# Kernel optimization log

Hardware: AMD Instinct MI355X
Metric: run time of the kernel (lower is better)

The kernel has to match this reference:

```python
import jax, jax.numpy as jnp
import numpy as np

DIM = 1024
HEADS = 16
HIDDEN = 4 * DIM


def layernorm(x, g, b, eps=1e-5):
    mu = jnp.mean(x, axis=-1, keepdims=True)
    var = jnp.mean(jnp.square(x - mu), axis=-1, keepdims=True)
    return (x - mu) * jax.lax.rsqrt(var + eps) * g + b


def setup_inputs() -> dict:
    key = jax.random.key(0)
    ks = jax.random.split(key, 8)
    s = DIM ** -0.5
    return {
        "x": jax.random.normal(ks[0], (2, 2048, DIM), dtype=jnp.float32),
        "ln1_g": jnp.ones((DIM,), jnp.float32),
        "ln1_b": jnp.zeros((DIM,), jnp.float32),
        "qkv_w": jax.random.normal(ks[1], (DIM, 3 * DIM), jnp.float32) * s,
        "proj_w": jax.random.normal(ks[2], (DIM, DIM), jnp.float32) * s,
        "proj_b": jnp.zeros((DIM,), jnp.float32),
        "ln2_g": jnp.ones((DIM,), jnp.float32),
        "ln2_b": jnp.zeros((DIM,), jnp.float32),
        "fc1_w": jax.random.normal(ks[3], (DIM, HIDDEN), jnp.float32) * s,
        "fc1_b": jnp.zeros((HIDDEN,), jnp.float32),
        "fc2_w": jax.random.normal(ks[4], (HIDDEN, DIM), jnp.float32) * (HIDDEN ** -0.5),
        "fc2_b": jnp.zeros((DIM,), jnp.float32),
    }


def block_fwd(x, ln1_g, ln1_b, qkv_w, proj_w, proj_b, ln2_g, ln2_b,
              fc1_w, fc1_b, fc2_w, fc2_b):
    B, N, C = x.shape
    H = HEADS
    Dh = C // H
    scale = Dh ** -0.5
    # --- attention branch (pre-norm) ---
    h = layernorm(x, ln1_g, ln1_b)
    qkv = h @ qkv_w                     # [B,N,3C] (no bias: qkv_bias=False)
    qkv = qkv.reshape(B, N, 3, H, Dh)
    q = qkv[:, :, 0].transpose(0, 2, 1, 3)   # [B,H,N,Dh]
    k = qkv[:, :, 1].transpose(0, 2, 1, 3)
    v = qkv[:, :, 2].transpose(0, 2, 1, 3)
    attn = jnp.einsum('bhqd,bhkd->bhqk', q, k) * scale
    attn = jax.nn.softmax(attn, axis=-1)
    o = jnp.einsum('bhqk,bhkd->bhqd', attn, v)
    o = o.transpose(0, 2, 1, 3).reshape(B, N, C)
    x = x + (o @ proj_w + proj_b)
    # --- MLP branch (pre-norm) ---
    h = layernorm(x, ln2_g, ln2_b)
    h = jax.nn.gelu(h @ fc1_w + fc1_b, approximate=False)  # torch nn.GELU = exact erf
    x = x + (h @ fc2_w + fc2_b)
    return x


def reference(x, ln1_g, ln1_b, qkv_w, proj_w, proj_b, ln2_g, ln2_b,
              fc1_w, fc1_b, fc2_w, fc2_b):
    return block_fwd(x, ln1_g, ln1_b, qkv_w, proj_w, proj_b, ln2_g, ln2_b,
                     fc1_w, fc1_b, fc2_w, fc2_b)
```

## Files before the change

### kernel.cpp

```cpp
#include <hip/hip_runtime.h>
#include <math.h>

typedef unsigned short u16;
typedef unsigned int u32;
typedef __attribute__((ext_vector_type(8))) short short8;
typedef __attribute__((ext_vector_type(4))) float f32x4;
typedef __attribute__((ext_vector_type(2))) u32 u32x2;
typedef __attribute__((ext_vector_type(4))) u32 u32x4;
typedef __attribute__((ext_vector_type(4))) u16 u16x4;

typedef __attribute__((address_space(1))) const void gmem_t;
typedef __attribute__((address_space(3))) void lmem_t;

__device__ __forceinline__ u16 f2bf(float f) {
  u32 u = __builtin_bit_cast(u32, f);
  u = u + 0x7fffu + ((u >> 16) & 1u);
  return (u16)(u >> 16);
}

__device__ __forceinline__ u32 cvt_pk_bf16(float a, float b) {
  u32 r;
  asm("v_cvt_pk_bf16_f32 %0, %1, %2" : "=v"(r) : "v"(a), "v"(b));
  return r;
}

__device__ __forceinline__ void g2l16(const void* g, void* l) {
  __builtin_amdgcn_global_load_lds((gmem_t*)g, (lmem_t*)l, 16, 0, 0);
}

template <int N> __device__ __forceinline__ void waitcnt_vm() {
  if constexpr (N == 0)      asm volatile("s_waitcnt vmcnt(0)" ::: "memory");
  else if constexpr (N == 4) asm volatile("s_waitcnt vmcnt(4)" ::: "memory");
  else if constexpr (N == 6) asm volatile("s_waitcnt vmcnt(6)" ::: "memory");
  else if constexpr (N == 8) asm volatile("s_waitcnt vmcnt(8)" ::: "memory");
  else static_assert(N == 0 || N == 4 || N == 6 || N == 8, "add literal");
}

__global__ __launch_bounds__(256) void wtrans_all(
    const float* __restrict__ qkvw, const float* __restrict__ projw,
    const float* __restrict__ fc1w, const float* __restrict__ fc2w,
    u16* __restrict__ o_qkv, u16* __restrict__ o_proj,
    u16* __restrict__ o_fc1, u16* __restrict__ o_fc2) {
  int id = (int)blockIdx.x;
  const float* in; u16* out; int R, C, bid;
  if (id < 768)       { in = qkvw;  out = o_qkv;  R = 1024; C = 3072; bid = id; }
  else if (id < 1024) { in = projw; out = o_proj; R = 1024; C = 1024; bid = id - 768; }
  else if (id < 2048) { in = fc1w;  out = o_fc1;  R = 1024; C = 4096; bid = id - 1024; }
  else                { in = fc2w;  out = o_fc2;  R = 4096; C = 1024; bid = id - 2048; }
  __shared__ float t[64][65];
  int tid = threadIdx.x;
  int nbx = C >> 6;
  int bx = bid % nbx, by = bid / nbx;
  int r0 = by << 6, c0 = bx << 6;
  int lr = tid >> 2, lc = (tid & 3) << 4;
  const float* src = in + (size_t)(r0 + lr) * C + c0 + lc;
#pragma unroll
  for (int j = 0; j < 4; ++j) {
    f32x4 v = *(const f32x4*)(src + j * 4);
    t[lr][lc + j * 4 + 0] = v.x; t[lr][lc + j * 4 + 1] = v.y;
    t[lr][lc + j * 4 + 2] = v.z; t[lr][lc + j * 4 + 3] = v.w;
  }
  __syncthreads();
  int oc = tid >> 2, orr = (tid & 3) << 4;
  u16* dst = out + (size_t)(c0 + oc) * R + r0 + orr;
  u32 u[8];
#pragma unroll
  for (int j = 0; j < 8; ++j)
    u[j] = (u32)f2bf(t[orr + 2 * j][oc]) | ((u32)f2bf(t[orr + 2 * j + 1][oc]) << 16);
  u32x4 v0; v0.x = u[0]; v0.y = u[1]; v0.z = u[2]; v0.w = u[3];
  u32x4 v1; v1.x = u[4]; v1.y = u[5]; v1.z = u[6]; v1.w = u[7];
  *(u32x4*)(dst) = v0;
  *(u32x4*)(dst + 8) = v1;
}

__global__ __launch_bounds__(256) void lnorm(const float* __restrict__ in,
                                             const float* __restrict__ gw,
                                             const float* __restrict__ bw,
                                             u16* __restrict__ out) {
  int r = blockIdx.x, tid = threadIdx.x;
  const f32x4 v = *((const f32x4*)(in + (size_t)r * 1024) + tid);
  float s = v.x + v.y + v.z + v.w;
  float ss = v.x * v.x + v.y * v.y + v.z * v.z + v.w * v.w;
#pragma unroll
  for (int o = 32; o >= 1; o >>= 1) { s += __shfl_xor(s, o); ss += __shfl_xor(ss, o); }
  __shared__ float red[8];
  int w = tid >> 6;
  if ((tid & 63) == 0) { red[w] = s; red[4 + w] = ss; }
  __syncthreads();
  s = red[0] + red[1] + red[2] + red[3];
  ss = red[4] + red[5] + red[6] + red[7];
  float mu = s * (1.0f / 1024.0f);
  float var = ss * (1.0f / 1024.0f) - mu * mu;
  float rstd = rsqrtf(var + 1e-5f);
  const f32x4 g4 = *((const f32x4*)gw + tid);
  const f32x4 b4 = *((const f32x4*)bw + tid);
  u16x4 o;
  o.x = f2bf((v.x - mu) * rstd * g4.x + b4.x);
  o.y = f2bf((v.y - mu) * rstd * g4.y + b4.y);
  o.z = f2bf((v.z - mu) * rstd * g4.z + b4.z);
  o.w = f2bf((v.w - mu) * rstd * g4.w + b4.w);
  *((u16x4*)(out + (size_t)r * 1024) + tid) = o;
}

template <int EPI, int BM, int BN>
__global__ __launch_bounds__(256, 2) void gemm_bt(
    const u16* __restrict__ A, const u16* __restrict__ BT, int M, int N, int K,
    const float* __restrict__ bias, const float* __restrict__ resid,
    float* __restrict__ fout, u16* __restrict__ bout,
    u16* __restrict__ bout2, u16* __restrict__ bout3) {
  constexpr int AIT = BM / 32, BIT = BN / 32;
  constexpr int L = AIT + BIT;
  constexpr int MR = BM / 32, NR = BN / 32;
  __shared__ __align__(16) u16 smA[2][BM * 64];
  __shared__ __align__(16) u16 smB[2][BN * 64];
  int tid = threadIdx.x;
  int w = tid >> 6, l = tid & 63, lq = l & 15, g = l >> 4;
  int nbx = N / BN;
  int t = (int)blockIdx.x;
  int cpx = (int)gridDim.x >> 3;
  t = (t & 7) * cpx + (t >> 3);
  int by = t / nbx, bx = t - by * nbx;
  long brow = (long)by * BM, bcol = (long)bx * BN;
  int wr = w >> 1, wc = w & 1;

  const u16* aS[AIT]; const u16* bS[BIT];
#pragma unroll
  for (int it = 0; it < AIT; ++it) {
    int p = it * 256 + tid;
    int row = p >> 3;
    int gc = (p & 7) ^ (row & 7);
    aS[it] = A + (size_t)(brow + row) * K + gc * 8;
  }
#pragma unroll
  for (int it = 0; it < BIT; ++it) {
    int p = it * 256 + tid;
    int row = p >> 3;
    int gc = (p & 7) ^ (row & 7);
    bS[it] = BT + (size_t)(bcol + row) * K + gc * 8;
  }
  auto STAGE = [&](int buf, int k0) {
#pragma unroll
    for (int it = 0; it < AIT; ++it) g2l16(aS[it] + k0, &smA[buf][it * 2048 + w * 512]);
#pragma unroll
    for (int it = 0; it < BIT; ++it) g2l16(bS[it] + k0, &smB[buf][it * 2048 + w * 512]);
  };

  f32x4 zero = {0.f, 0.f, 0.f, 0.f};
  f32x4 acc[MR][NR];
#pragma unroll
  for (int m = 0; m < MR; ++m)
#pragma unroll
    for (int n = 0; n < NR; ++n) acc[m][n] = zero;

  int NT = K >> 6;
  STAGE(0, 0);
  for (int tt = 0; tt < NT; ++tt) {
    int cur = tt & 1;
    int knext = ((tt + 1) == NT ? 0 : (tt + 1)) << 6;
    STAGE(cur ^ 1, knext);
    waitcnt_vm<L>();
    __builtin_amdgcn_s_barrier();
    asm volatile("" ::: "memory");

    const char* sA = (const char*)&smA[cur][0];
    const char* sB = (const char*)&smB[cur][0];
#pragma unroll
    for (int c = 0; c < 2; ++c) {
      short8 af[MR], bfb[NR];
#pragma unroll
      for (int m = 0; m < MR; ++m) {
        int r = wr * (BM / 2) + m * 16 + lq;
        af[m] = *(const short8*)(sA + r * 128 + ((g * 16 + c * 64) ^ ((r & 7) << 4)));
      }
#pragma unroll
      for (int n = 0; n < NR; ++n) {
        int r = wc * (BN / 2) + n * 16 + lq;
        bfb[n] = *(const short8*)(sB + r * 128 + ((g * 16 + c * 64) ^ ((r & 7) << 4)));
      }
#pragma unroll
      for (int m = 0; m < MR; ++m)
#pragma unroll
        for (int n = 0; n < NR; ++n)
          acc[m][n] = __builtin_amdgcn_mfma_f32_16x16x32_bf16(af[m], bfb[n], acc[m][n], 0, 0, 0);
    }
    asm volatile("" ::: "memory");
    __builtin_amdgcn_s_barrier();
  }
  waitcnt_vm<0>();

  long colbase = bcol + wc * (BN / 2);
#pragma unroll
  for (int m = 0; m < MR; ++m) {
#pragma unroll
    for (int n = 0; n < NR; ++n) {
      f32x4 v = acc[m][n];
      long col = colbase + n * 16 + lq;
      long row0 = brow + wr * (BM / 2) + m * 16 + g * 4;
      if constexpr (EPI == 0) {
        int part = (int)(bcol >> 10);
        long colq = col - ((long)part << 10);
        int hh = (int)(colq >> 6), d = (int)(colq & 63);
#pragma unroll
        for (int i = 0; i < 4; ++i) {
          long row = row0 + i;
          long b = row >> 11, nq = row & 2047;
          long bh = b * 16 + hh;
          u16 val = f2bf(v[i]);
          if (part == 0)      bout [(bh * 2048 + nq) * 64 + d] = val;
          else if (part == 1) bout2[(bh * 2048 + nq) * 64 + d] = val;
          else                bout3[(bh * 64 + d) * 2048 + nq] = val;
        }
      } else if constexpr (EPI == 1 || EPI == 3) {
        float bb = bias[col];
#pragma unroll
        for (int i = 0; i < 4; ++i) {
          long idx = (row0 + i) * N + col;
          fout[idx] = resid[idx] + v[i] + bb;
        }
      } else {
        float bb = bias[col];
#pragma unroll
        for (int i = 0; i < 4; ++i) {
          float xg = v[i] + bb;
          float ge = 0.5f * xg * (1.0f + erff(xg * 0.70710678118654752f));
          bout[(row0 + i) * N + col] = f2bf(ge);
        }
      }
    }
  }
}

__global__ __launch_bounds__(256, 4) void attn_fwd(const u16* __restrict__ qb,
                                                   const u16* __restrict__ kb,
                                                   const u16* __restrict__ vtb,
                                                   u16* __restrict__ ob) {
  __shared__ __align__(16) u16 kl[2][64 * 64];
  __shared__ __align__(16) u16 vl[2][64 * 64];
  __shared__ __align__(16) u16 pl[4][16 * 64];
  int tid = threadIdx.x;
  int w = tid >> 6, l = tid & 63, lq = l & 15, g = l >> 4;
  int bh = (int)blockIdx.x & 31;
  int qt = (int)blockIdx.x >> 5;

  const u16* qr = qb + ((size_t)bh * 2048 + qt * 64 + w * 16 + lq) * 64 + g * 8;
  short8 qf0 = *(const short8*)qr;
  short8 qf1 = *(const short8*)(qr + 32);

  const u16* kS[2]; const u16* vS[2];
#pragma unroll
  for (int it = 0; it < 2; ++it) {
    int p = it * 256 + tid;
    int row = p >> 3;
    int gc = (p & 7) ^ (row & 7);
    kS[it] = kb + ((size_t)bh * 2048 + row) * 64 + gc * 8;
    vS[it] = vtb + ((size_t)bh * 64 + row) * 2048 + gc * 8;
  }
  auto issue = [&](int buf, int kt0) {
#pragma unroll
    for (int it = 0; it < 2; ++it) {
      g2l16(kS[it] + (size_t)kt0 * 64, &kl[buf][it * 2048 + w * 512]);
      g2l16(vS[it] + kt0,              &vl[buf][it * 2048 + w * 512]);
    }
  };

  f32x4 zero = {0.f, 0.f, 0.f, 0.f};
  f32x4 accO[4] = {zero, zero, zero, zero};
  f32x4 accl = zero;
  const float sc = 0.125f * 1.44269504088896f;
  u32x4 ov; ov.x = ov.y = ov.z = ov.w = 0x3F803F80u;
  short8 onesf = __builtin_bit_cast(short8, ov);
  int plswz = (lq & 7) << 4;

  issue(0, 0);
  for (int t = 0; t < 32; ++t) {
    int cur = t & 1;
    issue(cur ^ 1, ((t + 1) & 31) << 6);
    waitcnt_vm<4>();
    __builtin_amdgcn_s_barrier();
    asm volatile("" ::: "memory");

    const char* klc = (const char*)&kl[cur][0];
    const char* vlc = (const char*)&vl[cur][0];

    f32x4 s[4];
    short8 ka0[4], ka1[4];
#pragma unroll
    for (int kt = 0; kt < 4; ++kt) {
      int r = kt * 16 + lq;
      ka0[kt] = *(const short8*)(klc + (r * 128 + ((g * 16) ^ ((r & 7) << 4))));
      ka1[kt] = *(const short8*)(klc + (r * 128 + ((g * 16 + 64) ^ ((r & 7) << 4))));
    }
    __builtin_amdgcn_s_setprio(1);
#pragma unroll
    for (int kt = 0; kt < 4; ++kt) {
      s[kt] = __builtin_amdgcn_mfma_f32_16x16x32_bf16(ka0[kt], qf0, zero, 0, 0, 0);
      s[kt] = __builtin_amdgcn_mfma_f32_16x16x32_bf16(ka1[kt], qf1, s[kt], 0, 0, 0);
    }
    __builtin_amdgcn_s_setprio(0);

    char* plw = (char*)&pl[w][0];
#pragma unroll
    for (int kt = 0; kt < 4; ++kt) {
      u32x2 uu;
      uu.x = cvt_pk_bf16(exp2f(s[kt][0] * sc - 12.0f), exp2f(s[kt][1] * sc - 12.0f));
      uu.y = cvt_pk_bf16(exp2f(s[kt][2] * sc - 12.0f), exp2f(s[kt][3] * sc - 12.0f));
      *(u32x2*)(plw + ((lq * 128 + kt * 32 + g * 8) ^ plswz)) = uu;
    }

#pragma unroll
    for (int c = 0; c < 2; ++c) {
      short8 pa = *(const short8*)(plw + ((lq * 128 + g * 16 + c * 64) ^ plswz));
      short8 vf[4];
#pragma unroll
      for (int dt = 0; dt < 4; ++dt) {
        int r = dt * 16 + lq;
        vf[dt] = *(const short8*)(vlc + (r * 128 + ((g * 16 + c * 64) ^ ((r & 7) << 4))));
      }
      __builtin_amdgcn_s_setprio(1);
#pragma unroll
      for (int dt = 0; dt < 4; ++dt)
        accO[dt] = __builtin_amdgcn_mfma_f32_16x16x32_bf16(pa, vf[dt], accO[dt], 0, 0, 0);
      accl = __builtin_amdgcn_mfma_f32_16x16x32_bf16(pa, onesf, accl, 0, 0, 0);
      __builtin_amdgcn_s_setprio(0);
    }
    asm volatile("" ::: "memory");
    __builtin_amdgcn_s_barrier();
  }
  waitcnt_vm<0>();

  float li[4];
#pragma unroll
  for (int i = 0; i < 4; ++i) li[i] = 1.0f / accl[i];
  int b = bh >> 4, h = bh & 15;
  long qbase = (long)qt * 64 + w * 16 + g * 4;
#pragma unroll
  for (int dt = 0; dt < 4; ++dt)
#pragma unroll
    for (int i = 0; i < 4; ++i) {
      long d = dt * 16 + lq;
      ob[((long)b * 2048 + qbase + i) * 1024 + h * 64 + d] = f2bf(accO[dt][i] * li[i]);
    }
}

extern "C" void kernel_launch(void* const* d_in, const int* in_sizes, int n_in,
                              void* d_out, int out_size, void* d_ws, size_t ws_size,
                              hipStream_t stream) {
  const float* x     = (const float*)d_in[0];
  const float* ln1g  = (const float*)d_in[1];
  const float* ln1b  = (const float*)d_in[2];
  const float* qkvw  = (const float*)d_in[3];
  const float* projw = (const float*)d_in[4];
  const float* projb = (const float*)d_in[5];
  const float* ln2g  = (const float*)d_in[6];
  const float* ln2b  = (const float*)d_in[7];
  const float* fc1w  = (const float*)d_in[8];
  const float* fc1b  = (const float*)d_in[9];
  const float* fc2w  = (const float*)d_in[10];
  const float* fc2b  = (const float*)d_in[11];
  char* ws = (char*)d_ws;
  u16* qkv_wt  = (u16*)(ws + 0);
  u16* proj_wt = (u16*)(ws + 6291456);
  u16* fc1_wt  = (u16*)(ws + 8388608);
  u16* fc2_wt  = (u16*)(ws + 16777216);
  u16* h       = (u16*)(ws + 25165824);
  u16* qbuf    = (u16*)(ws + 33554432);
  u16* kbuf    = (u16*)(ws + 41943040);
  u16* vtbuf   = (u16*)(ws + 50331648);
  u16* aout    = (u16*)(ws + 58720256);
  float* y1    = (float*)(ws + 67108864);
  u16* gbuf    = (u16*)(ws + 33554432);
  float* outp  = (float*)d_out;

  wtrans_all<<<3072, 256, 0, stream>>>(qkvw, projw, fc1w, fc2w,
                                       qkv_wt, proj_wt, fc1_wt, fc2_wt);

  lnorm<<<4096, 256, 0, stream>>>(x, ln1g, ln1b, h);
  gemm_bt<0, 128, 128><<<768, 256, 0, stream>>>(h, qkv_wt, 4096, 3072, 1024,
                                      nullptr, nullptr, nullptr, qbuf, kbuf, vtbuf);
  attn_fwd<<<1024, 256, 0, stream>>>(qbuf, kbuf, vtbuf, aout);
  gemm_bt<1, 64, 128><<<512, 256, 0, stream>>>(aout, proj_wt, 4096, 1024, 1024,
                                      projb, x, y1, nullptr, nullptr, nullptr);
  lnorm<<<4096, 256, 0, stream>>>(y1, ln2g, ln2b, h);
  gemm_bt<2, 128, 128><<<1024, 256, 0, stream>>>(h, fc1_wt, 4096, 4096, 1024,
                                       fc1b, nullptr, nullptr, gbuf, nullptr, nullptr);
  gemm_bt<3, 64, 128><<<512, 256, 0, stream>>>(gbuf, fc2_wt, 4096, 1024, 4096,
                                      fc2b, y1, outp, nullptr, nullptr, nullptr);
}
```

Measured before the change: 271.1 us.

## Rewrite attention with 32x32 MFMA, register-resident P, 128-query tiles

```diff
diff --git a/kernel.cpp b/kernel.cpp
--- a/kernel.cpp
+++ b/kernel.cpp
@@ -5,6 +5,7 @@
 typedef unsigned int u32;
 typedef __attribute__((ext_vector_type(8))) short short8;
 typedef __attribute__((ext_vector_type(4))) float f32x4;
+typedef __attribute__((ext_vector_type(16))) float f32x16;
 typedef __attribute__((ext_vector_type(2))) u32 u32x2;
 typedef __attribute__((ext_vector_type(4))) u32 u32x4;
 typedef __attribute__((ext_vector_type(4))) u16 u16x4;
@@ -230,21 +231,33 @@
   }
 }
 
-__global__ __launch_bounds__(256, 4) void attn_fwd(const u16* __restrict__ qb,
-                                                   const u16* __restrict__ kb,
+template <int BASE>
+__device__ __forceinline__ short8 mk_pfrag(const f32x16& s, float sc) {
+  u32 x = cvt_pk_bf16(exp2f(s[BASE + 0] * sc - 12.0f), exp2f(s[BASE + 1] * sc - 12.0f));
+  u32 y = cvt_pk_bf16(exp2f(s[BASE + 2] * sc - 12.0f), exp2f(s[BASE + 3] * sc - 12.0f));
+  u32 u = cvt_pk_bf16(exp2f(s[BASE + 4] * sc - 12.0f), exp2f(s[BASE + 5] * sc - 12.0f));
+  u32 v = cvt_pk_bf16(exp2f(s[BASE + 6] * sc - 12.0f), exp2f(s[BASE + 7] * sc - 12.0f));
+  asm("v_permlane32_swap_b32 %0, %1" : "+v"(x), "+v"(u));
+  asm("v_permlane32_swap_b32 %0, %1" : "+v"(y), "+v"(v));
+  u32x4 f; f.x = x; f.y = y; f.z = u; f.w = v;
+  return __builtin_bit_cast(short8, f);
+}
+
+__global__ __launch_bounds__(256, 2) void attn_fwd(const u16* __restrict__ qb,
+                                                   const u16* __restrict__ kbuf,
                                                    const u16* __restrict__ vtb,
                                                    u16* __restrict__ ob) {
   __shared__ __align__(16) u16 kl[2][64 * 64];
   __shared__ __align__(16) u16 vl[2][64 * 64];
-  __shared__ __align__(16) u16 pl[4][16 * 64];
   int tid = threadIdx.x;
-  int w = tid >> 6, l = tid & 63, lq = l & 15, g = l >> 4;
+  int w = tid >> 6, l = tid & 63, q32 = l & 31, hi = l >> 5;
   int bh = (int)blockIdx.x & 31;
   int qt = (int)blockIdx.x >> 5;
 
-  const u16* qr = qb + ((size_t)bh * 2048 + qt * 64 + w * 16 + lq) * 64 + g * 8;
-  short8 qf0 = *(const short8*)qr;
-  short8 qf1 = *(const short8*)(qr + 32);
+  const u16* qp = qb + ((size_t)bh * 2048 + qt * 128 + w * 32 + q32) * 64 + hi * 8;
+  short8 qf[4];
+#pragma unroll
+  for (int kc = 0; kc < 4; ++kc) qf[kc] = *(const short8*)(qp + kc * 16);
 
   const u16* kS[2]; const u16* vS[2];
 #pragma unroll
@@ -252,7 +265,7 @@
     int p = it * 256 + tid;
     int row = p >> 3;
     int gc = (p & 7) ^ (row & 7);
-    kS[it] = kb + ((size_t)bh * 2048 + row) * 64 + gc * 8;
+    kS[it] = kbuf + ((size_t)bh * 2048 + row) * 64 + gc * 8;
     vS[it] = vtb + ((size_t)bh * 64 + row) * 2048 + gc * 8;
   }
   auto issue = [&](int buf, int kt0) {
@@ -263,13 +276,12 @@
     }
   };
 
-  f32x4 zero = {0.f, 0.f, 0.f, 0.f};
-  f32x4 accO[4] = {zero, zero, zero, zero};
-  f32x4 accl = zero;
+  f32x16 z16 = {0,0,0,0,0,0,0,0,0,0,0,0,0,0,0,0};
+  f32x16 accO0 = z16, accO1 = z16, accl = z16;
   const float sc = 0.125f * 1.44269504088896f;
   u32x4 ov; ov.x = ov.y = ov.z = ov.w = 0x3F803F80u;
   short8 onesf = __builtin_bit_cast(short8, ov);
-  int plswz = (lq & 7) << 4;
+  int swz = (q32 & 7) << 4;
 
   issue(0, 0);
   for (int t = 0; t < 32; ++t) {
@@ -282,64 +294,58 @@
     const char* klc = (const char*)&kl[cur][0];
     const char* vlc = (const char*)&vl[cur][0];
 
-    f32x4 s[4];
-    short8 ka0[4], ka1[4];
-#pragma unroll
-    for (int kt = 0; kt < 4; ++kt) {
-      int r = kt * 16 + lq;
-      ka0[kt] = *(const short8*)(klc + (r * 128 + ((g * 16) ^ ((r & 7) << 4))));
-      ka1[kt] = *(const short8*)(klc + (r * 128 + ((g * 16 + 64) ^ ((r & 7) << 4))));
-    }
+    f32x16 s0 = z16, s1 = z16;
     __builtin_amdgcn_s_setprio(1);
 #pragma unroll
-    for (int kt = 0; kt < 4; ++kt) {
-      s[kt] = __builtin_amdgcn_mfma_f32_16x16x32_bf16(ka0[kt], qf0, zero, 0, 0, 0);
-      s[kt] = __builtin_amdgcn_mfma_f32_16x16x32_bf16(ka1[kt], qf1, s[kt], 0, 0, 0);
+    for (int kc = 0; kc < 4; ++kc) {
+      short8 k0 = *(const short8*)(klc + (q32 * 128 +        ((kc * 32 + hi * 16) ^ swz)));
+      short8 k1 = *(const short8*)(klc + ((32 + q32) * 128 + ((kc * 32 + hi * 16) ^ swz)));
+      s0 = __builtin_amdgcn_mfma_f32_32x32x16_bf16(k0, qf[kc], s0, 0, 0, 0);
+      s1 = __builtin_amdgcn_mfma_f32_32x32x16_bf16(k1, qf[kc], s1, 0, 0, 0);
     }
     __builtin_amdgcn_s_setprio(0);
 
-    char* plw = (char*)&pl[w][0];
-#pragma unroll
-    for (int kt = 0; kt < 4; ++kt) {
-      u32x2 uu;
-      uu.x = cvt_pk_bf16(exp2f(s[kt][0] * sc - 12.0f), exp2f(s[kt][1] * sc - 12.0f));
-      uu.y = cvt_pk_bf16(exp2f(s[kt][2] * sc - 12.0f), exp2f(s[kt][3] * sc - 12.0f));
-      *(u32x2*)(plw + ((lq * 128 + kt * 32 + g * 8) ^ plswz)) = uu;
-    }
-
-#pragma unroll
-    for (int c = 0; c < 2; ++c) {
-      short8 pa = *(const short8*)(plw + ((lq * 128 + g * 16 + c * 64) ^ plswz));
-      short8 vf[4];
-#pragma unroll
-      for (int dt = 0; dt < 4; ++dt) {
-        int r = dt * 16 + lq;
-        vf[dt] = *(const short8*)(vlc + (r * 128 + ((g * 16 + c * 64) ^ ((r & 7) << 4))));
-      }
-      __builtin_amdgcn_s_setprio(1);
-#pragma unroll
-      for (int dt = 0; dt < 4; ++dt)
-        accO[dt] = __builtin_amdgcn_mfma_f32_16x16x32_bf16(pa, vf[dt], accO[dt], 0, 0, 0);
-      accl = __builtin_amdgcn_mfma_f32_16x16x32_bf16(pa, onesf, accl, 0, 0, 0);
-      __builtin_amdgcn_s_setprio(0);
-    }
+    short8 pf0 = mk_pfrag<0>(s0, sc);
+    short8 pf1 = mk_pfrag<8>(s0, sc);
+    short8 pf2 = mk_pfrag<0>(s1, sc);
+    short8 pf3 = mk_pfrag<8>(s1, sc);
+
+    short8 va0[4], va1[4];
+#pragma unroll
+    for (int c = 0; c < 4; ++c) {
+      va0[c] = *(const short8*)(vlc + (q32 * 128 +        ((c * 32 + hi * 16) ^ swz)));
+      va1[c] = *(const short8*)(vlc + ((32 + q32) * 128 + ((c * 32 + hi * 16) ^ swz)));
+    }
+    __builtin_amdgcn_s_setprio(1);
+    accO0 = __builtin_amdgcn_mfma_f32_32x32x16_bf16(va0[0], pf0, accO0, 0, 0, 0);
+    accO1 = __builtin_amdgcn_mfma_f32_32x32x16_bf16(va1[0], pf0, accO1, 0, 0, 0);
+    accl  = __builtin_amdgcn_mfma_f32_32x32x16_bf16(onesf,  pf0, accl,  0, 0, 0);
+    accO0 = __builtin_amdgcn_mfma_f32_32x32x16_bf16(va0[1], pf1, accO0, 0, 0, 0);
+    accO1 = __builtin_amdgcn_mfma_f32_32x32x16_bf16(va1[1], pf1, accO1, 0, 0, 0);
+    accl  = __builtin_amdgcn_mfma_f32_32x32x16_bf16(onesf,  pf1, accl,  0, 0, 0);
+    accO0 = __builtin_amdgcn_mfma_f32_32x32x16_bf16(va0[2], pf2, accO0, 0, 0, 0);
+    accO1 = __builtin_amdgcn_mfma_f32_32x32x16_bf16(va1[2], pf2, accO1, 0, 0, 0);
+    accl  = __builtin_amdgcn_mfma_f32_32x32x16_bf16(onesf,  pf2, accl,  0, 0, 0);
+    accO0 = __builtin_amdgcn_mfma_f32_32x32x16_bf16(va0[3], pf3, accO0, 0, 0, 0);
+    accO1 = __builtin_amdgcn_mfma_f32_32x32x16_bf16(va1[3], pf3, accO1, 0, 0, 0);
+    accl  = __builtin_amdgcn_mfma_f32_32x32x16_bf16(onesf,  pf3, accl,  0, 0, 0);
+    __builtin_amdgcn_s_setprio(0);
+
     asm volatile("" ::: "memory");
     __builtin_amdgcn_s_barrier();
   }
   waitcnt_vm<0>();
 
-  float li[4];
-#pragma unroll
-  for (int i = 0; i < 4; ++i) li[i] = 1.0f / accl[i];
+  float li = 1.0f / accl[0];
   int b = bh >> 4, h = bh & 15;
-  long qbase = (long)qt * 64 + w * 16 + g * 4;
-#pragma unroll
-  for (int dt = 0; dt < 4; ++dt)
-#pragma unroll
-    for (int i = 0; i < 4; ++i) {
-      long d = dt * 16 + lq;
-      ob[((long)b * 2048 + qbase + i) * 1024 + h * 64 + d] = f2bf(accO[dt][i] * li[i]);
-    }
+  long q = (long)qt * 128 + w * 32 + q32;
+  u16* obase = ob + ((long)b * 2048 + q) * 1024 + h * 64;
+#pragma unroll
+  for (int j = 0; j < 8; ++j) {
+    int d = ((2 * j) & 3) + 8 * (j >> 1) + 4 * hi;
+    *(u32*)(obase + d)      = cvt_pk_bf16(accO0[2 * j] * li, accO0[2 * j + 1] * li);
+    *(u32*)(obase + 32 + d) = cvt_pk_bf16(accO1[2 * j] * li, accO1[2 * j + 1] * li);
+  }
 }
 
 extern "C" void kernel_launch(void* const* d_in, const int* in_sizes, int n_in,
@@ -377,7 +383,7 @@
   lnorm<<<4096, 256, 0, stream>>>(x, ln1g, ln1b, h);
   gemm_bt<0, 128, 128><<<768, 256, 0, stream>>>(h, qkv_wt, 4096, 3072, 1024,
                                       nullptr, nullptr, nullptr, qbuf, kbuf, vtbuf);
-  attn_fwd<<<1024, 256, 0, stream>>>(qbuf, kbuf, vtbuf, aout);
+  attn_fwd<<<512, 256, 0, stream>>>(qbuf, kbuf, vtbuf, aout);
   gemm_bt<1, 64, 128><<<512, 256, 0, stream>>>(aout, proj_wt, 4096, 1024, 1024,
                                       projb, x, y1, nullptr, nullptr, nullptr);
   lnorm<<<4096, 256, 0, stream>>>(y1, ln2g, ln2b, h);
```

Result: faster. 263.5 us (-2.8%).
